# Optimization experiments

Measured on AMD Instinct MI355X. Metric: run time of the kernel, lower is better.

Reference implementation:

```python
import jax, jax.numpy as jnp
import numpy as np

EMBED_DIM = 1024
NUM_HEADS = 16
HEAD_DIM = EMBED_DIM // NUM_HEADS
EPS = 1e-5


def setup_inputs() -> dict:
    key = jax.random.key(0)
    ks = jax.random.split(key, 14)
    B, S, E = 2, 2048, EMBED_DIM
    s = 1.0 / np.sqrt(E)
    inp = {
        "x": jax.random.normal(ks[0], (B, S, E), dtype=jnp.float32),
        "Wq": jax.random.normal(ks[1], (E, E), dtype=jnp.float32) * s,
        "bq": jax.random.normal(ks[2], (E,), dtype=jnp.float32) * 0.01,
        "Wk": jax.random.normal(ks[3], (E, E), dtype=jnp.float32) * s,
        "bk": jax.random.normal(ks[4], (E,), dtype=jnp.float32) * 0.01,
        "Wv": jax.random.normal(ks[5], (E, E), dtype=jnp.float32) * s,
        "bv": jax.random.normal(ks[6], (E,), dtype=jnp.float32) * 0.01,
        "Wo": jax.random.normal(ks[7], (E, E), dtype=jnp.float32) * s,
        "bo": jax.random.normal(ks[8], (E,), dtype=jnp.float32) * 0.01,
        "qn_w": jnp.ones((HEAD_DIM,), jnp.float32) + 0.1 * jax.random.normal(ks[9], (HEAD_DIM,), jnp.float32),
        "qn_b": 0.1 * jax.random.normal(ks[10], (HEAD_DIM,), jnp.float32),
        "kn_w": jnp.ones((HEAD_DIM,), jnp.float32) + 0.1 * jax.random.normal(ks[11], (HEAD_DIM,), jnp.float32),
        "kn_b": 0.1 * jax.random.normal(ks[12], (HEAD_DIM,), jnp.float32),
    }
    return inp


def _layernorm(t, w, b):
    # normalize over last axis (head_dim), matching eqx.nn.LayerNorm(eps=1e-5)
    mu = jnp.mean(t, axis=-1, keepdims=True)
    var = jnp.mean(jnp.square(t - mu), axis=-1, keepdims=True)
    return (t - mu) * jax.lax.rsqrt(var + EPS) * w + b


def reference(x, Wq, bq, Wk, bk, Wv, bv, Wo, bo, qn_w, qn_b, kn_w, kn_b):
    B, S, E = x.shape
    H, D = NUM_HEADS, HEAD_DIM
    q = (x @ Wq.T + bq).reshape(B, S, H, D)
    k = (x @ Wk.T + bk).reshape(B, S, H, D)
    v = (x @ Wv.T + bv).reshape(B, S, H, D)
    q = _layernorm(q, qn_w, qn_b)
    k = _layernorm(k, kn_w, kn_b)
    scale = D ** (-0.5)
    # [B,H,S,S] score matrix (faithful to naive implementation)
    scores = jnp.einsum("bqhd,bkhd->bhqk", q, k) * scale
    attn = jax.nn.softmax(scores, axis=-1)
    out = jnp.einsum("bhqk,bkhd->bqhd", attn, v).reshape(B, S, E)
    return out @ Wo.T + bo
```

## Files before the change

kernel.cpp:

```cpp
#include <hip/hip_runtime.h>
#include <stdint.h>


typedef __bf16 bf16_t;
typedef __bf16 bf16x8 __attribute__((ext_vector_type(8)));
typedef __bf16 bf16x4 __attribute__((ext_vector_type(4)));
typedef __bf16 bf16x2 __attribute__((ext_vector_type(2)));
typedef float f32x4 __attribute__((ext_vector_type(4)));
typedef float f32x16 __attribute__((ext_vector_type(16)));
typedef uint32_t u32x4 __attribute__((ext_vector_type(4)));

#define S_LEN 2048
#define QSCALE 0.1803368801f

__device__ __forceinline__ void load_lds16(const void* g, void* l) {
  __builtin_amdgcn_global_load_lds((__attribute__((address_space(1))) void*)g,
                                   (__attribute__((address_space(3))) void*)l,
                                   16, 0, 0);
}

__device__ __forceinline__ f32x4 mfma16(bf16x8 a, bf16x8 b, f32x4 c) {
  return __builtin_amdgcn_mfma_f32_16x16x32_bf16(a, b, c, 0, 0, 0);
}

__device__ __forceinline__ f32x16 mfma32(bf16x8 a, bf16x8 b, f32x16 c) {
  return __builtin_amdgcn_mfma_f32_32x32x16_bf16(a, b, c, 0, 0, 0);
}

__device__ __forceinline__ uint32_t pk_bf16(float a, float b) {
  bf16x2 v; v[0] = (bf16_t)a; v[1] = (bf16_t)b;
  return __builtin_bit_cast(uint32_t, v);
}

__device__ __forceinline__ void plswap(uint32_t& a, uint32_t& b) {
  asm volatile("v_permlane32_swap_b32 %0, %1" : "+v"(a), "+v"(b));
}

__global__ void cvt_all(const float* __restrict__ x, const float* __restrict__ Wq,
                        const float* __restrict__ Wk, const float* __restrict__ Wv,
                        const float* __restrict__ Wo,
                        bf16_t* __restrict__ xb, bf16_t* __restrict__ Wb,
                        bf16_t* __restrict__ Wob) {
  const int bid = blockIdx.x;
  const float* src; bf16_t* dst; int idx;
  if (bid < 4096) { src = x; dst = xb; idx = bid; }
  else {
    const int r = bid - 4096, rg = r >> 10;
    idx = r & 1023;
    if (rg == 0)      { src = Wq; dst = Wb; }
    else if (rg == 1) { src = Wk; dst = Wb + (1 << 20); }
    else if (rg == 2) { src = Wv; dst = Wb + (2 << 20); }
    else              { src = Wo; dst = Wob; }
  }
  const int i = (idx * 256 + threadIdx.x) * 4;
  float4 v = *reinterpret_cast<const float4*>(src + i);
  bf16x4 o;
  o[0] = (bf16_t)v.x; o[1] = (bf16_t)v.y; o[2] = (bf16_t)v.z; o[3] = (bf16_t)v.w;
  *reinterpret_cast<bf16x4*>(dst + i) = o;
}

__launch_bounds__(256, 2)
__global__ void gemm_qkv_ln(const bf16_t* __restrict__ A, const bf16_t* __restrict__ Bt,
                            const float* __restrict__ bq, const float* __restrict__ bk,
                            const float* __restrict__ bv,
                            const float* __restrict__ qnw, const float* __restrict__ qnb,
                            const float* __restrict__ knw, const float* __restrict__ knb,
                            bf16_t* __restrict__ Qb, bf16_t* __restrict__ Kb,
                            bf16_t* __restrict__ Vt) {
  __shared__ alignas(16) bf16_t As[2][128 * 32];
  __shared__ alignas(16) bf16_t Bs[2][128 * 32];
  const int t = threadIdx.x;
  const int orig = blockIdx.y * 24 + blockIdx.x;
  const int logical = (orig & 7) * 96 + (orig >> 3);
  const int bn = logical % 24, bm = logical / 24;
  const int w = t >> 6, lane = t & 63;
  const int wr = w >> 1, wc = w & 1;
  const int lg = lane >> 4, lr = lane & 15;

  f32x4 acc[4][4] = {};
  const int srow = t >> 2;
  const int scol = (t & 3) << 3;
  const bf16_t* ga = A + ((size_t)(bm * 128 + srow) << 10) + scol;
  const bf16_t* gb = Bt + ((size_t)(bn * 128 + srow) << 10) + scol;

#define GSTAGE(buf, k0)                                        \
  {                                                            \
    load_lds16(ga + (k0),         &As[buf][t * 8]);            \
    load_lds16(ga + 65536 + (k0), &As[buf][2048 + t * 8]);     \
    load_lds16(gb + (k0),         &Bs[buf][t * 8]);            \
    load_lds16(gb + 65536 + (k0), &Bs[buf][2048 + t * 8]);     \
  }

  GSTAGE(0, 0);
  __syncthreads();
  for (int it = 0; it < 32; ++it) {
    const int cur = it & 1;
    if (it < 31) GSTAGE(cur ^ 1, (it + 1) << 5);
    bf16x8 af[4], bfr[4];
#pragma unroll
    for (int mt = 0; mt < 4; ++mt)
      af[mt] = *reinterpret_cast<const bf16x8*>(&As[cur][((wr * 64 + mt * 16 + lr) << 5) + lg * 8]);
#pragma unroll
    for (int nt = 0; nt < 4; ++nt)
      bfr[nt] = *reinterpret_cast<const bf16x8*>(&Bs[cur][((wc * 64 + nt * 16 + lr) << 5) + lg * 8]);
#pragma unroll
    for (int mt = 0; mt < 4; ++mt)
#pragma unroll
      for (int nt = 0; nt < 4; ++nt)
        acc[mt][nt] = mfma16(af[mt], bfr[nt], acc[mt][nt]);
    __syncthreads();
  }
#undef GSTAGE

  const int nbase = bn * 128 + wc * 64;
  const int region = nbase >> 10;
  const int h = (nbase & 1023) >> 6;

  if (region == 2) {
    char* Vb = reinterpret_cast<char*>((w < 2) ? &As[w][0] : &Bs[w - 2][0]);
#pragma unroll
    for (int mt = 0; mt < 4; ++mt)
#pragma unroll
      for (int nt = 0; nt < 4; ++nt) {
        const int d = nt * 16 + lr;
        const float bvd = bv[h * 64 + d];
        const int slot = (mt * 2 + (lg >> 1)) ^ (d & 7);
        uint2 pr;
        pr.x = pk_bf16(acc[mt][nt][0] + bvd, acc[mt][nt][1] + bvd);
        pr.y = pk_bf16(acc[mt][nt][2] + bvd, acc[mt][nt][3] + bvd);
        *reinterpret_cast<uint2*>(Vb + d * 128 + slot * 16 + (lg & 1) * 8) = pr;
      }
    asm volatile("s_waitcnt lgkmcnt(0)" ::: "memory");
    const int s0 = bm * 128 + wr * 64;
    const int bb = s0 >> 11;
    const int sl = s0 & 2047;
#pragma unroll
    for (int it2 = 0; it2 < 8; ++it2) {
      const int d = it2 * 8 + (lane >> 3);
      const int ch = lane & 7;
      bf16x8 vv8 = *reinterpret_cast<const bf16x8*>(Vb + d * 128 + ((ch ^ (d & 7)) << 4));
      *reinterpret_cast<bf16x8*>(
          Vt + (((size_t)((bb * 16 + h) * 64 + d)) << 11) + sl + ch * 8) = vv8;
    }
  } else {
    const float* bias = region ? bk : bq;
    const float* lw = region ? knw : qnw;
    const float* lb = region ? knb : qnb;
    const float osc = region ? 1.0f : QSCALE;
    bf16_t* Outp = region ? Kb : Qb;
#pragma unroll
    for (int mt = 0; mt < 4; ++mt)
#pragma unroll
      for (int r = 0; r < 4; ++r) {
        const int gm = bm * 128 + wr * 64 + mt * 16 + lg * 4 + r;
        const int b = gm >> 11, s = gm & 2047;
        float vv[4], sum = 0.f, sumsq = 0.f;
#pragma unroll
        for (int nt = 0; nt < 4; ++nt) {
          const int d = nt * 16 + lr;
          vv[nt] = acc[mt][nt][r] + bias[h * 64 + d];
          sum += vv[nt];
          sumsq += vv[nt] * vv[nt];
        }
#pragma unroll
        for (int mk = 1; mk < 16; mk <<= 1) {
          sum += __shfl_xor(sum, mk);
          sumsq += __shfl_xor(sumsq, mk);
        }
        const float mean = sum * (1.f / 64.f);
        const float var = sumsq * (1.f / 64.f) - mean * mean;
        const float rstd = rsqrtf(var + 1e-5f);
        const size_t rowoff = ((size_t)((b * 16 + h) * 2048 + s)) << 6;
#pragma unroll
        for (int nt = 0; nt < 4; ++nt) {
          const int d = nt * 16 + lr;
          float y = ((vv[nt] - mean) * rstd * lw[d] + lb[d]) * osc;
          Outp[rowoff + d] = (bf16_t)y;
        }
      }
  }
}

__launch_bounds__(256, 2)
__global__ void gemm_out(const bf16_t* __restrict__ A, const bf16_t* __restrict__ Bt,
                         const float* __restrict__ bo, float* __restrict__ dout) {
  __shared__ alignas(16) bf16_t As[2][64 * 32];
  __shared__ alignas(16) bf16_t Bs[2][128 * 32];
  const int t = threadIdx.x;
  const int orig = blockIdx.y * 8 + blockIdx.x;
  const int logical = (orig & 7) * 64 + (orig >> 3);
  const int bn = logical & 7, bm = logical >> 3;
  const int w = t >> 6, lane = t & 63;
  const int wr = w >> 1, wc = w & 1;
  const int lg = lane >> 4, lr = lane & 15;

  f32x4 acc[2][4] = {};
  const int srow = t >> 2;
  const int scol = (t & 3) << 3;
  const bf16_t* ga = A + ((size_t)(bm * 64 + srow) << 10) + scol;
  const bf16_t* gb = Bt + ((size_t)(bn * 128 + srow) << 10) + scol;

#define OSTAGE(buf, k0)                                        \
  {                                                            \
    load_lds16(ga + (k0),         &As[buf][t * 8]);            \
    load_lds16(gb + (k0),         &Bs[buf][t * 8]);            \
    load_lds16(gb + 65536 + (k0), &Bs[buf][2048 + t * 8]);     \
  }

  OSTAGE(0, 0);
  __syncthreads();
  for (int it = 0; it < 32; ++it) {
    const int cur = it & 1;
    if (it < 31) OSTAGE(cur ^ 1, (it + 1) << 5);
    bf16x8 af[2], bfr[4];
#pragma unroll
    for (int mt = 0; mt < 2; ++mt)
      af[mt] = *reinterpret_cast<const bf16x8*>(&As[cur][((wr * 32 + mt * 16 + lr) << 5) + lg * 8]);
#pragma unroll
    for (int nt = 0; nt < 4; ++nt)
      bfr[nt] = *reinterpret_cast<const bf16x8*>(&Bs[cur][((wc * 64 + nt * 16 + lr) << 5) + lg * 8]);
#pragma unroll
    for (int mt = 0; mt < 2; ++mt)
#pragma unroll
      for (int nt = 0; nt < 4; ++nt)
        acc[mt][nt] = mfma16(af[mt], bfr[nt], acc[mt][nt]);
    __syncthreads();
  }
#undef OSTAGE

#pragma unroll
  for (int mt = 0; mt < 2; ++mt)
#pragma unroll
    for (int r = 0; r < 4; ++r) {
      const int gm = bm * 64 + wr * 32 + mt * 16 + lg * 4 + r;
#pragma unroll
      for (int nt = 0; nt < 4; ++nt) {
        const int gn = bn * 128 + wc * 64 + nt * 16 + lr;
        dout[((size_t)gm << 10) + gn] = acc[mt][nt][r] + bo[gn];
      }
    }
}

template <int NSPLIT>
__launch_bounds__(256, 4)
__global__ void attn_kernel(const bf16_t* __restrict__ Qb, const bf16_t* __restrict__ Kb,
                            const bf16_t* __restrict__ Vt, bf16_t* __restrict__ Og,
                            bf16_t* __restrict__ Op, float* __restrict__ Lp) {
  __shared__ alignas(16) bf16_t KVs[4][64 * 64];

  const int t = threadIdx.x;
  const int w = t >> 6, lane = t & 63;
  const int lq = lane & 31;
  const int hi = lane >> 5;
  const int orig = (blockIdx.z * 32 + blockIdx.y) * 16 + blockIdx.x;
  const int logical = (orig & 7) * (64 * NSPLIT) + (orig >> 3);
  const int qt = logical & 15;
  const int bh = (logical >> 4) & 31;
  const int z = (NSPLIT == 1) ? 0 : (logical >> 9);
  const int b = bh >> 4, h = bh & 15;
  const int q0 = qt * 128 + w * 32;
  const int ntiles = 32 / NSPLIT;

  bf16x8 qf[4];
  {
    const bf16_t* qp = Qb + (((size_t)bh * S_LEN + q0 + lq) << 6) + hi * 8;
#pragma unroll
    for (int c = 0; c < 4; ++c)
      qf[c] = *reinterpret_cast<const bf16x8*>(qp + c * 16);
  }

  f32x16 oacc0 = {}, oacc1 = {}, lacc = {};

  const int krow = (t >> 1) & 63;
  const int kch = ((t >> 7) << 1) | (t & 1);
  const bf16_t* kbase = Kb + (((size_t)bh * S_LEN) << 6) + krow * 64 + kch * 8;
  const bf16_t* vbase = Vt + ((size_t)bh << 17) + krow * S_LEN + kch * 8;

#define STAGE(buf, jt)                                                       \
  {                                                                          \
    const bf16_t* kb_ = kbase + (((size_t)(jt)) << 12);                      \
    const bf16_t* vb_ = vbase + (jt) * 64;                                   \
    load_lds16(kb_,      &KVs[buf][t * 8]);                                  \
    load_lds16(kb_ + 32, &KVs[buf][2048 + t * 8]);                           \
    load_lds16(vb_,      &KVs[2 + (buf)][t * 8]);                            \
    load_lds16(vb_ + 32, &KVs[2 + (buf)][2048 + t * 8]);                     \
  }

  STAGE(0, z * ntiles);
  __syncthreads();

  for (int j = 0; j < ntiles; ++j) {
    const int cur = j & 1;
    if (j < ntiles - 1) STAGE(cur ^ 1, z * ntiles + j + 1);

    f32x16 s0 = {}, s1 = {};
    const bf16_t* kr = &KVs[cur][lq * 16 + hi * 8];
    __builtin_amdgcn_s_setprio(1);
#pragma unroll
    for (int c = 0; c < 4; ++c) {
      bf16x8 kf = *reinterpret_cast<const bf16x8*>(kr + c * 1024);
      s0 = mfma32(kf, qf[c], s0);
    }
#pragma unroll
    for (int c = 0; c < 4; ++c) {
      bf16x8 kf = *reinterpret_cast<const bf16x8*>(kr + 512 + c * 1024);
      s1 = mfma32(kf, qf[c], s1);
    }
    __builtin_amdgcn_s_setprio(0);

    f32x16 p0, p1;
#pragma unroll
    for (int i = 0; i < 16; ++i) p0[i] = __builtin_amdgcn_exp2f(s0[i]);
#pragma unroll
    for (int i = 0; i < 16; ++i) p1[i] = __builtin_amdgcn_exp2f(s1[i]);
    lacc += p0;
    lacc += p1;

    const bf16_t* vr = &KVs[2 + cur][lq * 16 + hi * 8];
    __builtin_amdgcn_s_setprio(1);
#pragma unroll
    for (int c = 0; c < 4; ++c) {
      const f32x16 ph = (c < 2) ? p0 : p1;
      const int cl = c & 1;
      uint32_t w00 = pk_bf16(ph[8 * cl + 0], ph[8 * cl + 1]);
      uint32_t w01 = pk_bf16(ph[8 * cl + 2], ph[8 * cl + 3]);
      uint32_t w10 = pk_bf16(ph[8 * cl + 4], ph[8 * cl + 5]);
      uint32_t w11 = pk_bf16(ph[8 * cl + 6], ph[8 * cl + 7]);
      plswap(w00, w10);
      plswap(w01, w11);
      u32x4 pw = {w00, w01, w10, w11};
      bf16x8 pf = __builtin_bit_cast(bf16x8, pw);
      {
        bf16x8 vf = *reinterpret_cast<const bf16x8*>(vr + c * 1024);
        oacc0 = mfma32(vf, pf, oacc0);
      }
      {
        bf16x8 vf = *reinterpret_cast<const bf16x8*>(vr + 512 + c * 1024);
        oacc1 = mfma32(vf, pf, oacc1);
      }
    }
    __builtin_amdgcn_s_setprio(0);
    __syncthreads();
  }

  float l_;
  {
    float sv[8];
#pragma unroll
    for (int i = 0; i < 8; ++i) sv[i] = lacc[i] + lacc[i + 8];
#pragma unroll
    for (int s2 = 4; s2 >= 1; s2 >>= 1)
#pragma unroll
      for (int i = 0; i < s2; ++i) sv[i] += sv[i + s2];
    l_ = sv[0] + __shfl_xor(sv[0], 32);
  }

  {
    bf16_t* Os = &KVs[0][0] + w * 2048;
    const float inv = (NSPLIT == 1) ? __builtin_amdgcn_rcpf(l_) : 1.0f;
#pragma unroll
    for (int dh = 0; dh < 2; ++dh) {
      const f32x16 oa = dh ? oacc1 : oacc0;
#pragma unroll
      for (int g = 0; g < 8; ++g) {
        const int reg = g * 2;
        const int dl = (reg & 3) + 8 * (reg >> 2) + 4 * hi;
        const int d = dh * 32 + dl;
        const uint32_t wv = pk_bf16(oa[reg] * inv, oa[reg + 1] * inv);
        const int byte = lq * 128 + ((((d >> 3) ^ (lq & 7))) << 4) + ((d & 7) << 1);
        *reinterpret_cast<uint32_t*>(reinterpret_cast<char*>(Os) + byte) = wv;
      }
    }
    if (NSPLIT == 2 && lane < 32)
      Lp[(size_t)(z * 32 + bh) * 2048 + q0 + lq] = l_;
#pragma unroll
    for (int it = 0; it < 4; ++it) {
      const int q = it * 8 + (lane >> 3);
      const int ch = lane & 7;
      bf16x8 ov = *reinterpret_cast<const bf16x8*>(
          reinterpret_cast<char*>(Os) + q * 128 + ((ch ^ (q & 7)) << 4));
      if constexpr (NSPLIT == 1) {
        const size_t gaddr = (((size_t)(b * S_LEN + q0 + q)) << 10) + h * 64 + ch * 8;
        *reinterpret_cast<bf16x8*>(Og + gaddr) = ov;
      } else {
        const size_t rowoff = ((size_t)((z * 32 + bh) * 2048 + q0 + q)) << 6;
        *reinterpret_cast<bf16x8*>(Op + rowoff + ch * 8) = ov;
      }
    }
  }
#undef STAGE
}

__global__ void attn_combine(const bf16_t* __restrict__ Op, const float* __restrict__ Lp,
                             bf16_t* __restrict__ Ob) {
  const int gid = blockIdx.x * 256 + threadIdx.x;
  const int row = gid >> 3, ch = gid & 7;
  const bf16_t* o1 = Op + ((size_t)row << 6) + ch * 8;
  const bf16_t* o2 = o1 + (1u << 22);
  const float inv = 1.f / (Lp[row] + Lp[(1u << 16) + row]);
  bf16x8 v1 = *reinterpret_cast<const bf16x8*>(o1);
  bf16x8 v2 = *reinterpret_cast<const bf16x8*>(o2);
  bf16x8 o;
#pragma unroll
  for (int i = 0; i < 8; ++i) o[i] = (bf16_t)(((float)v1[i] + (float)v2[i]) * inv);
  const int bh = row >> 11, s = row & 2047;
  const int b = bh >> 4, h = bh & 15;
  *reinterpret_cast<bf16x8*>(Ob + (((size_t)(b * S_LEN + s)) << 10) + h * 64 + ch * 8) = o;
}

extern "C" void kernel_launch(void* const* d_in, const int* in_sizes, int n_in,
                              void* d_out, int out_size, void* d_ws, size_t ws_size,
                              hipStream_t stream) {
  const float* x = (const float*)d_in[0];
  const float* Wq = (const float*)d_in[1];
  const float* bq = (const float*)d_in[2];
  const float* Wk = (const float*)d_in[3];
  const float* bk = (const float*)d_in[4];
  const float* Wv = (const float*)d_in[5];
  const float* bv = (const float*)d_in[6];
  const float* Wo = (const float*)d_in[7];
  const float* bo = (const float*)d_in[8];
  const float* qnw = (const float*)d_in[9];
  const float* qnb = (const float*)d_in[10];
  const float* knw = (const float*)d_in[11];
  const float* knb = (const float*)d_in[12];
  float* out = (float*)d_out;

  uint8_t* ws = (uint8_t*)d_ws;
  bf16_t* xb = (bf16_t*)(ws + 0);
  bf16_t* Wb = (bf16_t*)(ws + 8388608);
  bf16_t* Wob = (bf16_t*)(ws + 14680064);
  bf16_t* Qb = (bf16_t*)(ws + 16777216);
  bf16_t* Kb = (bf16_t*)(ws + 25165824);
  bf16_t* Vt = (bf16_t*)(ws + 33554432);
  bf16_t* Ob = (bf16_t*)(ws + 41943040);
  bf16_t* Opart = (bf16_t*)(ws + 50331648);
  float*  Lpart = (float*)(ws + 67108864);
  const bool split = ws_size >= 67633152ull;

  cvt_all<<<8192, 256, 0, stream>>>(x, Wq, Wk, Wv, Wo, xb, Wb, Wob);

  gemm_qkv_ln<<<dim3(24, 32), 256, 0, stream>>>(xb, Wb, bq, bk, bv, qnw, qnb, knw, knb,
                                                Qb, Kb, Vt);
  if (split) {
    attn_kernel<2><<<dim3(16, 32, 2), 256, 0, stream>>>(Qb, Kb, Vt, Ob, Opart, Lpart);
    attn_combine<<<2048, 256, 0, stream>>>(Opart, Lpart, Ob);
  } else {
    attn_kernel<1><<<dim3(16, 32, 1), 256, 0, stream>>>(Qb, Kb, Vt, Ob, Opart, Lpart);
  }
  gemm_out<<<dim3(8, 64), 256, 0, stream>>>(Ob, Wob, bo, out);
}
```

Measured before the change: 117.3 us.

## Enlarge QKV GEMM tiles to 256x256 with triple-buffered LDS pipeline

Each QKV projection block now computes a 256x256 output tile with 512 threads instead of 128x128 with 256 threads. The K loop uses a three-stage LDS ring prefetched two steps ahead, split into two MFMA half-phases separated by explicit barriers, with raised wave priority around the MFMA bursts. This is meant to improve operand reuse and overlap global loads with compute. The cost is that the grid drops from 768 to 192 blocks, fewer than the CU count, so parts of the GPU may sit idle. The LayerNorm and V-transpose epilogues are adapted to the larger tile.

```diff
diff --git a/kernel.cpp b/kernel.cpp
--- a/kernel.cpp
+++ b/kernel.cpp
@@ -59,7 +59,7 @@
   *reinterpret_cast<bf16x4*>(dst + i) = o;
 }
 
-__launch_bounds__(256, 2)
+__launch_bounds__(512, 2)
 __global__ void gemm_qkv_ln(const bf16_t* __restrict__ A, const bf16_t* __restrict__ Bt,
                             const float* __restrict__ bq, const float* __restrict__ bk,
                             const float* __restrict__ bv,
@@ -67,80 +67,119 @@
                             const float* __restrict__ knw, const float* __restrict__ knb,
                             bf16_t* __restrict__ Qb, bf16_t* __restrict__ Kb,
                             bf16_t* __restrict__ Vt) {
-  __shared__ alignas(16) bf16_t As[2][128 * 32];
-  __shared__ alignas(16) bf16_t Bs[2][128 * 32];
+  __shared__ alignas(16) bf16_t S[3 * 16384];
   const int t = threadIdx.x;
-  const int orig = blockIdx.y * 24 + blockIdx.x;
-  const int logical = (orig & 7) * 96 + (orig >> 3);
-  const int bn = logical % 24, bm = logical / 24;
-  const int w = t >> 6, lane = t & 63;
-  const int wr = w >> 1, wc = w & 1;
+  const int wid = t >> 6, lane = t & 63;
+  const int wr = wid >> 2, wcn = wid & 3;
   const int lg = lane >> 4, lr = lane & 15;
-
-  f32x4 acc[4][4] = {};
-  const int srow = t >> 2;
-  const int scol = (t & 3) << 3;
-  const bf16_t* ga = A + ((size_t)(bm * 128 + srow) << 10) + scol;
-  const bf16_t* gb = Bt + ((size_t)(bn * 128 + srow) << 10) + scol;
-
-#define GSTAGE(buf, k0)                                        \
-  {                                                            \
-    load_lds16(ga + (k0),         &As[buf][t * 8]);            \
-    load_lds16(ga + 65536 + (k0), &As[buf][2048 + t * 8]);     \
-    load_lds16(gb + (k0),         &Bs[buf][t * 8]);            \
-    load_lds16(gb + 65536 + (k0), &Bs[buf][2048 + t * 8]);     \
-  }
-
-  GSTAGE(0, 0);
-  __syncthreads();
-  for (int it = 0; it < 32; ++it) {
-    const int cur = it & 1;
-    if (it < 31) GSTAGE(cur ^ 1, (it + 1) << 5);
-    bf16x8 af[4], bfr[4];
-#pragma unroll
-    for (int mt = 0; mt < 4; ++mt)
-      af[mt] = *reinterpret_cast<const bf16x8*>(&As[cur][((wr * 64 + mt * 16 + lr) << 5) + lg * 8]);
+  const int orig = blockIdx.x;
+  const int swz = (orig & 7) * 24 + (orig >> 3);
+  const int bm = swz / 12, bn = swz % 12;
+
+  const bf16_t* gA = A + (size_t)(bm * 256 + (t & 127)) * 1024 + ((t >> 7) << 3);
+  const bf16_t* gB = Bt + (size_t)(bn * 256 + (t & 127)) * 1024 + ((t >> 7) << 3);
+
+  f32x4 acc[8][4] = {};
+  bf16x8 bfr[4], af[4];
+
+  const int aoff = wr * 4096 + lg * 1024 + lr * 8;
+  const int boff = 8192 + (wcn >> 1) * 4096 + lg * 1024 + (wcn & 1) * 512 + lr * 8;
+
+#define ST(bufx, ktx, op, hh)                                                  \
+  load_lds16(((op) ? gB : gA) + (hh) * 131072 + (ktx) * 32,                    \
+             &S[(bufx) * 16384 + (op) * 8192 + (hh) * 4096 + t * 8])
+
+  ST(0, 0, 0, 0); ST(0, 0, 0, 1); ST(0, 0, 1, 0); ST(0, 0, 1, 1);
+  ST(1, 1, 0, 0); ST(1, 1, 0, 1); ST(1, 1, 1, 0); ST(1, 1, 1, 1);
+
+  int buf = 0, buf2 = 2;
+  for (int kt = 0; kt < 32; ++kt) {
+    const int ks2 = (kt + 2 < 32) ? kt + 2 : 31;
+    const int sbase = buf * 16384;
+    asm volatile("s_waitcnt vmcnt(4)" ::: "memory");
+    __builtin_amdgcn_sched_barrier(0);
+    __builtin_amdgcn_s_barrier();
+    __builtin_amdgcn_sched_barrier(0);
 #pragma unroll
     for (int nt = 0; nt < 4; ++nt)
-      bfr[nt] = *reinterpret_cast<const bf16x8*>(&Bs[cur][((wc * 64 + nt * 16 + lr) << 5) + lg * 8]);
-#pragma unroll
-    for (int mt = 0; mt < 4; ++mt)
+      bfr[nt] = *reinterpret_cast<const bf16x8*>(&S[sbase + boff + nt * 128]);
+#pragma unroll
+    for (int m2 = 0; m2 < 4; ++m2)
+      af[m2] = *reinterpret_cast<const bf16x8*>(&S[sbase + aoff + m2 * 128]);
+    ST(buf2, ks2, 0, 0);
+    ST(buf2, ks2, 0, 1);
+    __builtin_amdgcn_s_barrier();
+    asm volatile("s_waitcnt lgkmcnt(0)" ::: "memory");
+    __builtin_amdgcn_sched_barrier(0);
+    __builtin_amdgcn_s_setprio(1);
+#pragma unroll
+    for (int m2 = 0; m2 < 4; ++m2)
 #pragma unroll
       for (int nt = 0; nt < 4; ++nt)
-        acc[mt][nt] = mfma16(af[mt], bfr[nt], acc[mt][nt]);
-    __syncthreads();
-  }
-#undef GSTAGE
-
-  const int nbase = bn * 128 + wc * 64;
+        acc[m2][nt] = mfma16(af[m2], bfr[nt], acc[m2][nt]);
+    __builtin_amdgcn_s_setprio(0);
+    __builtin_amdgcn_s_barrier();
+#pragma unroll
+    for (int m2 = 0; m2 < 4; ++m2)
+      af[m2] = *reinterpret_cast<const bf16x8*>(&S[sbase + aoff + (4 + m2) * 128]);
+    ST(buf2, ks2, 1, 0);
+    ST(buf2, ks2, 1, 1);
+    __builtin_amdgcn_s_barrier();
+    asm volatile("s_waitcnt lgkmcnt(0)" ::: "memory");
+    __builtin_amdgcn_sched_barrier(0);
+    __builtin_amdgcn_s_setprio(1);
+#pragma unroll
+    for (int m2 = 0; m2 < 4; ++m2)
+#pragma unroll
+      for (int nt = 0; nt < 4; ++nt)
+        acc[4 + m2][nt] = mfma16(af[m2], bfr[nt], acc[4 + m2][nt]);
+    __builtin_amdgcn_s_setprio(0);
+    __builtin_amdgcn_s_barrier();
+    buf = (buf == 2) ? 0 : buf + 1;
+    buf2 = (buf2 == 2) ? 0 : buf2 + 1;
+  }
+#undef ST
+
+  const int nbase = bn * 256 + wcn * 64;
   const int region = nbase >> 10;
   const int h = (nbase & 1023) >> 6;
 
   if (region == 2) {
-    char* Vb = reinterpret_cast<char*>((w < 2) ? &As[w][0] : &Bs[w - 2][0]);
-#pragma unroll
-    for (int mt = 0; mt < 4; ++mt)
-#pragma unroll
-      for (int nt = 0; nt < 4; ++nt) {
-        const int d = nt * 16 + lr;
-        const float bvd = bv[h * 64 + d];
-        const int slot = (mt * 2 + (lg >> 1)) ^ (d & 7);
-        uint2 pr;
-        pr.x = pk_bf16(acc[mt][nt][0] + bvd, acc[mt][nt][1] + bvd);
-        pr.y = pk_bf16(acc[mt][nt][2] + bvd, acc[mt][nt][3] + bvd);
-        *reinterpret_cast<uint2*>(Vb + d * 128 + slot * 16 + (lg & 1) * 8) = pr;
-      }
-    asm volatile("s_waitcnt lgkmcnt(0)" ::: "memory");
-    const int s0 = bm * 128 + wr * 64;
-    const int bb = s0 >> 11;
-    const int sl = s0 & 2047;
-#pragma unroll
-    for (int it2 = 0; it2 < 8; ++it2) {
-      const int d = it2 * 8 + (lane >> 3);
-      const int ch = lane & 7;
-      bf16x8 vv8 = *reinterpret_cast<const bf16x8*>(Vb + d * 128 + ((ch ^ (d & 7)) << 4));
-      *reinterpret_cast<bf16x8*>(
-          Vt + (((size_t)((bb * 16 + h) * 64 + d)) << 11) + sl + ch * 8) = vv8;
+    __syncthreads();
+    char* Vb = reinterpret_cast<char*>(&S[wid * 4096]);
+    const int s0g = bm * 256 + wr * 128;
+    const int bb = s0g >> 11;
+    const int sl = s0g & 2047;
+#pragma unroll
+    for (int bt = 0; bt < 2; ++bt) {
+#pragma unroll
+      for (int m3 = 0; m3 < 4; ++m3) {
+        const int mt = bt * 4 + m3;
+#pragma unroll
+        for (int nt = 0; nt < 4; ++nt) {
+          const int d = nt * 16 + lr;
+          const float bvd = bv[h * 64 + d];
+          const int slot = (m3 * 2 + (lg >> 1)) ^ (d & 7);
+          uint2 pr;
+          pr.x = pk_bf16(acc[mt][nt][0] + bvd, acc[mt][nt][1] + bvd);
+          pr.y = pk_bf16(acc[mt][nt][2] + bvd, acc[mt][nt][3] + bvd);
+          *reinterpret_cast<uint2*>(Vb + d * 128 + slot * 16 + (lg & 1) * 8) = pr;
+        }
+      }
+      asm volatile("s_waitcnt lgkmcnt(0)" ::: "memory");
+      __builtin_amdgcn_sched_barrier(0);
+#pragma unroll
+      for (int it2 = 0; it2 < 8; ++it2) {
+        const int d = it2 * 8 + (lane >> 3);
+        const int ch = lane & 7;
+        bf16x8 vv8 = *reinterpret_cast<const bf16x8*>(Vb + d * 128 + ((ch ^ (d & 7)) << 4));
+        *reinterpret_cast<bf16x8*>(
+            Vt + (((size_t)((bb * 16 + h) * 64 + d)) << 11) + sl + bt * 64 + ch * 8) = vv8;
+      }
+      if (bt == 0) {
+        asm volatile("s_waitcnt lgkmcnt(0)" ::: "memory");
+        __builtin_amdgcn_sched_barrier(0);
+      }
     }
   } else {
     const float* bias = region ? bk : bq;
@@ -149,10 +188,10 @@
     const float osc = region ? 1.0f : QSCALE;
     bf16_t* Outp = region ? Kb : Qb;
 #pragma unroll
-    for (int mt = 0; mt < 4; ++mt)
+    for (int mt = 0; mt < 8; ++mt)
 #pragma unroll
       for (int r = 0; r < 4; ++r) {
-        const int gm = bm * 128 + wr * 64 + mt * 16 + lg * 4 + r;
+        const int gm = bm * 256 + wr * 128 + mt * 16 + lg * 4 + r;
         const int b = gm >> 11, s = gm & 2047;
         float vv[4], sum = 0.f, sumsq = 0.f;
 #pragma unroll
@@ -440,8 +479,8 @@
 
   cvt_all<<<8192, 256, 0, stream>>>(x, Wq, Wk, Wv, Wo, xb, Wb, Wob);
 
-  gemm_qkv_ln<<<dim3(24, 32), 256, 0, stream>>>(xb, Wb, bq, bk, bv, qnw, qnb, knw, knb,
-                                                Qb, Kb, Vt);
+  gemm_qkv_ln<<<192, 512, 0, stream>>>(xb, Wb, bq, bk, bv, qnw, qnb, knw, knb,
+                                       Qb, Kb, Vt);
   if (split) {
     attn_kernel<2><<<dim3(16, 32, 2), 256, 0, stream>>>(Qb, Kb, Vt, Ob, Opart, Lpart);
     attn_combine<<<2048, 256, 0, stream>>>(Opart, Lpart, Ob);
```

Result: slower. 127.6 us (+8.8%).
